# Performance work log

Measured on AMD Instinct MI355X. Metric: run time of the kernel, lower is better.

The kernel has to match this reference:

```python
import jax, jax.numpy as jnp
import numpy as np

N = 50000
GAMMA = 0.1

def spmm(row, col, val, x):
    # sparse [N,N] @ dense [N,D] via gather + segment-sum over destination rows
    return jax.ops.segment_sum(val[:, None] * x[col], row, num_segments=N)

def setup_inputs() -> dict:
    key = jax.random.key(0)
    ks = jax.random.split(key, 16)
    E, EK, F, H, C = 800000, 1000000, 512, 128, 40
    return {
        "fea": jax.random.normal(ks[0], (N, F), jnp.float32),
        "adj_row": jax.random.randint(ks[1], (E,), 0, N),
        "adj_col": jax.random.randint(ks[2], (E,), 0, N),
        "adj_val": jax.random.uniform(ks[3], (E,), jnp.float32),
        "knn_row": jax.random.randint(ks[4], (EK,), 0, N),
        "knn_col": jax.random.randint(ks[5], (EK,), 0, N),
        "knn_val": jax.random.uniform(ks[6], (EK,), jnp.float32),
        "W1": jax.random.normal(ks[7], (F, H), jnp.float32) * (1.0 / np.sqrt(F)),
        "b1": jnp.zeros((H,), jnp.float32),
        "W2": jax.random.normal(ks[8], (H, C), jnp.float32) * (1.0 / np.sqrt(H)),
        "b2": jnp.zeros((C,), jnp.float32),
        "score1": jax.random.normal(ks[9], (F, 1), jnp.float32),
        "score2": jax.random.normal(ks[10], (H, 1), jnp.float32),
        "sbias1": jnp.zeros((1,), jnp.float32),
        "sbias2": jnp.zeros((1,), jnp.float32),
        "Dk1": jax.random.normal(ks[11], (F, 1), jnp.float32),
        "Dk2": jax.random.normal(ks[12], (H, 1), jnp.float32),
        "Dbias1": jnp.zeros((1,), jnp.float32),
        "Dbias2": jnp.zeros((1,), jnp.float32),
    }

def simpgcn_layer(x, W, b, s_w, s_b, d_w, d_b, adj_row, adj_col, adj_val, knn_row, knn_col, knn_val):
    support = x @ W                     # [N, Dout] shared across the 3 adjacencies
    h_adj = spmm(adj_row, adj_col, adj_val, support) + b
    h_knn = spmm(knn_row, knn_col, knn_val, support) + b
    h_id = support + b                  # identity adjacency: spmm(I, support)
    s = jax.nn.sigmoid(x @ s_w + s_b)   # [N,1] learned self-loop gate
    Dk = x @ d_w + d_b                  # [N,1]
    return s * h_adj + (1.0 - s) * h_knn + GAMMA * Dk * h_id

def reference(fea, adj_row, adj_col, adj_val, knn_row, knn_col, knn_val,
              W1, b1, W2, b2, score1, score2, sbias1, sbias2,
              Dk1, Dk2, Dbias1, Dbias2):
    x = simpgcn_layer(fea, W1, b1, score1, sbias1, Dk1, Dbias1,
                      adj_row, adj_col, adj_val, knn_row, knn_col, knn_val)
    embedding = x  # dropout is identity in eval mode
    x = simpgcn_layer(x, W2, b2, score2, sbias2, Dk2, Dbias2,
                      adj_row, adj_col, adj_val, knn_row, knn_col, knn_val)
    return jax.nn.log_softmax(x, axis=1), embedding
```

## Files before the change

kernel.cpp:

```cpp
#include <hip/hip_runtime.h>
#include <hip/hip_bf16.h>
#include <cstdint>

#define GAMMA 0.1f
#define CAP 64
#define OVF_CAP 8192

typedef unsigned int  uint32;
typedef unsigned short ushort16;
typedef float f32x4 __attribute__((ext_vector_type(4)));
typedef __bf16 bf16x8 __attribute__((ext_vector_type(8)));

union U16x8 { uint4 u4; bf16x8 bv; };

static __device__ __forceinline__ ushort16 f2bf(float f) {
    union { float f; uint32 u; } x; x.f = f;
    uint32 r = (x.u + 0x7FFFu + ((x.u >> 16) & 1u)) >> 16;
    return (ushort16)r;
}
static __device__ __forceinline__ uint32 pack2bf(float lo, float hi) {
    return (uint32)f2bf(lo) | ((uint32)f2bf(hi) << 16);
}
static __device__ __forceinline__ float bflo(uint32 u) { return __uint_as_float(u << 16); }
static __device__ __forceinline__ float bfhi(uint32 u) { return __uint_as_float(u & 0xFFFF0000u); }

__global__ __launch_bounds__(256) void prep_wt(const float* __restrict__ W1,
                                               const float* __restrict__ W2,
                                               ushort16* __restrict__ W1bt,
                                               ushort16* __restrict__ W2bt) {
    int t = blockIdx.x * 256 + threadIdx.x;
    if (t < 128 * 512) { int c = t >> 9, k = t & 511; W1bt[t] = f2bf(W1[k * 128 + c]); }
    if (t < 48 * 128)  { int c = t >> 7, k = t & 127; W2bt[t] = f2bf(c < 40 ? W2[k * 40 + c] : 0.f); }
}

__global__ __launch_bounds__(256) void gemm1_scatter(
    const float* __restrict__ A, const ushort16* __restrict__ Bt,
    const float* __restrict__ s1w, const float* __restrict__ d1w,
    const float* __restrict__ s1b, const float* __restrict__ d1b,
    ushort16* __restrict__ Cb, float* __restrict__ s_out, float* __restrict__ dk_out,
    int M, int mgrid,
    const int* __restrict__ arow_, const int* __restrict__ acol_, const float* __restrict__ aval_, int E,
    const int* __restrict__ krow_, const int* __restrict__ kcol_, const float* __restrict__ kval_, int EK,
    int* __restrict__ cnt, int N,
    uint32* __restrict__ packed_a, uint32* __restrict__ packed_k,
    uint2* __restrict__ ovf_a, uint2* __restrict__ ovf_k) {
    int bid = blockIdx.x;
    if (bid >= mgrid) {
        int i = (bid - mgrid) * 256 + threadIdx.x;
        if (i < E) {
            int r = arow_[i];
            uint32 rec = ((uint32)acol_[i] << 16) | (uint32)f2bf(aval_[i]);
            int p = atomicAdd(&cnt[r], 1);
            if (p < CAP) packed_a[(size_t)r * CAP + p] = rec;
            else { int q = atomicAdd(&cnt[2 * N], 1); if (q < OVF_CAP) ovf_a[q] = make_uint2((uint32)r, rec); }
        }
        if (i < EK) {
            int r = krow_[i];
            uint32 rec = ((uint32)kcol_[i] << 16) | (uint32)f2bf(kval_[i]);
            int p = atomicAdd(&cnt[N + r], 1);
            if (p < CAP) packed_k[(size_t)r * CAP + p] = rec;
            else { int q = atomicAdd(&cnt[2 * N + 1], 1); if (q < OVF_CAP) ovf_k[q] = make_uint2((uint32)r, rec); }
        }
        return;
    }
    int w = threadIdx.x >> 6, lane = threadIdx.x & 63;
    int row16 = lane & 15, kc = lane >> 4;
    int wrow0 = bid * 64 + w * 16;
    int r = wrow0 + row16;
    int rc = min(r, M - 1);
    const float* arow = A + (size_t)rc * 512;

    f32x4 acc[8];
    #pragma unroll
    for (int c = 0; c < 8; ++c) acc[c] = (f32x4){0.f, 0.f, 0.f, 0.f};
    float sdot = 0.f, ddot = 0.f;

    for (int ks = 0; ks < 16; ++ks) {
        int kb = ks * 32 + kc * 8;
        float4 a0 = *reinterpret_cast<const float4*>(arow + kb);
        float4 a1 = *reinterpret_cast<const float4*>(arow + kb + 4);
        float4 sw0 = *reinterpret_cast<const float4*>(s1w + kb);
        float4 sw1 = *reinterpret_cast<const float4*>(s1w + kb + 4);
        float4 dw0 = *reinterpret_cast<const float4*>(d1w + kb);
        float4 dw1 = *reinterpret_cast<const float4*>(d1w + kb + 4);
        sdot += a0.x * sw0.x + a0.y * sw0.y + a0.z * sw0.z + a0.w * sw0.w +
                a1.x * sw1.x + a1.y * sw1.y + a1.z * sw1.z + a1.w * sw1.w;
        ddot += a0.x * dw0.x + a0.y * dw0.y + a0.z * dw0.z + a0.w * dw0.w +
                a1.x * dw1.x + a1.y * dw1.y + a1.z * dw1.z + a1.w * dw1.w;
        U16x8 ua;
        ua.u4 = make_uint4(pack2bf(a0.x, a0.y), pack2bf(a0.z, a0.w),
                           pack2bf(a1.x, a1.y), pack2bf(a1.z, a1.w));
        #pragma unroll
        for (int c = 0; c < 8; ++c) {
            U16x8 ub;
            ub.u4 = *reinterpret_cast<const uint4*>(Bt + (size_t)(c * 16 + row16) * 512 + kb);
            acc[c] = __builtin_amdgcn_mfma_f32_16x16x32_bf16(ua.bv, ub.bv, acc[c], 0, 0, 0);
        }
    }

    sdot += __shfl_xor(sdot, 16); sdot += __shfl_xor(sdot, 32);
    ddot += __shfl_xor(ddot, 16); ddot += __shfl_xor(ddot, 32);
    if (kc == 0 && r < M) {
        s_out[r] = 1.f / (1.f + __expf(-(sdot + s1b[0])));
        dk_out[r] = ddot + d1b[0];
    }

    #pragma unroll
    for (int c = 0; c < 8; ++c) {
        #pragma unroll
        for (int i = 0; i < 4; ++i) {
            int orow = wrow0 + (lane >> 4) * 4 + i;
            if (orow < M) Cb[(size_t)orow * 128 + c * 16 + row16] = f2bf(acc[c][i]);
        }
    }
}

__global__ __launch_bounds__(256) void gemm2_mfma(const ushort16* __restrict__ Ab,
                                                  const ushort16* __restrict__ Bt,
                                                  float* __restrict__ C,
                                                  ushort16* __restrict__ Cb,
                                                  int M) {
    int w = threadIdx.x >> 6, lane = threadIdx.x & 63;
    int row16 = lane & 15, kc = lane >> 4;
    int wrow0 = blockIdx.x * 64 + w * 16;
    int r = wrow0 + row16;
    int rc = min(r, M - 1);

    f32x4 acc[3];
    #pragma unroll
    for (int c = 0; c < 3; ++c) acc[c] = (f32x4){0.f, 0.f, 0.f, 0.f};

    #pragma unroll
    for (int ks = 0; ks < 4; ++ks) {
        int kb = ks * 32 + kc * 8;
        U16x8 ua;
        ua.u4 = *reinterpret_cast<const uint4*>(Ab + (size_t)rc * 128 + kb);
        #pragma unroll
        for (int c = 0; c < 3; ++c) {
            U16x8 ub;
            ub.u4 = *reinterpret_cast<const uint4*>(Bt + (size_t)(c * 16 + row16) * 128 + kb);
            acc[c] = __builtin_amdgcn_mfma_f32_16x16x32_bf16(ua.bv, ub.bv, acc[c], 0, 0, 0);
        }
    }

    #pragma unroll
    for (int c = 0; c < 3; ++c) {
        int col = c * 16 + row16;
        #pragma unroll
        for (int i = 0; i < 4; ++i) {
            int orow = wrow0 + (lane >> 4) * 4 + i;
            if (orow < M && col < 40) {
                C[(size_t)orow * 40 + col] = acc[c][i];
                Cb[(size_t)orow * 40 + col] = f2bf(acc[c][i]);
            }
        }
    }
}

__global__ __launch_bounds__(256) void spmm_combine1(
    const int* __restrict__ cnt,
    const uint32* __restrict__ packed_a, const uint32* __restrict__ packed_k,
    const uint2* __restrict__ ovf_a, const uint2* __restrict__ ovf_k,
    const ushort16* __restrict__ supb, const float* __restrict__ s, const float* __restrict__ dk,
    const float* __restrict__ b1,
    const float* __restrict__ s2w, const float* __restrict__ d2w,
    const float* __restrict__ s2b, const float* __restrict__ d2b,
    float* __restrict__ emb, ushort16* __restrict__ embb,
    float* __restrict__ s_out, float* __restrict__ dk_out, int N) {
    int w = threadIdx.x >> 6, lane = threadIdx.x & 63;
    int r = blockIdx.x * 4 + w;
    if (r >= N) return;
    const uint32* su = (const uint32*)supb;

    float a0 = 0.f, a1 = 0.f, k0 = 0.f, k1 = 0.f;
    {
        const uint32* pa = packed_a + (size_t)r * CAP;
        int d = min(cnt[r], CAP);
        int e = 0;
        for (; e + 2 <= d; e += 2) {
            uint32 r0 = pa[e], r1 = pa[e + 1];
            float v0 = bflo(r0), v1 = bflo(r1);
            uint32 u0 = su[((size_t)(r0 >> 16) << 6) + lane];
            uint32 u1 = su[((size_t)(r1 >> 16) << 6) + lane];
            a0 += v0 * bflo(u0) + v1 * bflo(u1);
            a1 += v0 * bfhi(u0) + v1 * bfhi(u1);
        }
        if (e < d) {
            uint32 r0 = pa[e];
            float v0 = bflo(r0);
            uint32 u0 = su[((size_t)(r0 >> 16) << 6) + lane];
            a0 += v0 * bflo(u0); a1 += v0 * bfhi(u0);
        }
    }
    {
        const uint32* pk = packed_k + (size_t)r * CAP;
        int d = min(cnt[N + r], CAP);
        int e = 0;
        for (; e + 2 <= d; e += 2) {
            uint32 r0 = pk[e], r1 = pk[e + 1];
            float v0 = bflo(r0), v1 = bflo(r1);
            uint32 u0 = su[((size_t)(r0 >> 16) << 6) + lane];
            uint32 u1 = su[((size_t)(r1 >> 16) << 6) + lane];
            k0 += v0 * bflo(u0) + v1 * bflo(u1);
            k1 += v0 * bfhi(u0) + v1 * bfhi(u1);
        }
        if (e < d) {
            uint32 r0 = pk[e];
            float v0 = bflo(r0);
            uint32 u0 = su[((size_t)(r0 >> 16) << 6) + lane];
            k0 += v0 * bflo(u0); k1 += v0 * bfhi(u0);
        }
    }
    int nova = min(cnt[2 * N], OVF_CAP);
    for (int i = 0; i < nova; ++i) {
        uint2 t = ovf_a[i];
        if ((int)t.x == r) {
            float v = bflo(t.y);
            uint32 u = su[((size_t)(t.y >> 16) << 6) + lane];
            a0 += v * bflo(u); a1 += v * bfhi(u);
        }
    }
    int novk = min(cnt[2 * N + 1], OVF_CAP);
    for (int i = 0; i < novk; ++i) {
        uint2 t = ovf_k[i];
        if ((int)t.x == r) {
            float v = bflo(t.y);
            uint32 u = su[((size_t)(t.y >> 16) << 6) + lane];
            k0 += v * bflo(u); k1 += v * bfhi(u);
        }
    }

    float si = s[r];
    float g = GAMMA * dk[r];
    uint32 ui = su[((size_t)r << 6) + lane];
    int c0i = lane * 2, c1i = lane * 2 + 1;
    float o0 = si * a0 + (1.f - si) * k0 + g * bflo(ui) + b1[c0i] * (1.f + g);
    float o1 = si * a1 + (1.f - si) * k1 + g * bfhi(ui) + b1[c1i] * (1.f + g);

    *reinterpret_cast<float2*>(emb + (size_t)r * 128 + c0i) = make_float2(o0, o1);
    ((uint32*)embb)[((size_t)r << 6) + lane] = pack2bf(o0, o1);

    float as = o0 * s2w[c0i] + o1 * s2w[c1i];
    float ad = o0 * d2w[c0i] + o1 * d2w[c1i];
    #pragma unroll
    for (int off = 32; off; off >>= 1) {
        as += __shfl_xor(as, off);
        ad += __shfl_xor(ad, off);
    }
    if (lane == 0) {
        s_out[r] = 1.f / (1.f + __expf(-(as + s2b[0])));
        dk_out[r] = ad + d2b[0];
    }
}

__global__ __launch_bounds__(256) void spmm_combine2_lsm(
    const int* __restrict__ cnt,
    const uint32* __restrict__ packed_a, const uint32* __restrict__ packed_k,
    const uint2* __restrict__ ovf_a, const uint2* __restrict__ ovf_k,
    const ushort16* __restrict__ supb, const float* __restrict__ supf,
    const float* __restrict__ s, const float* __restrict__ dk,
    const float* __restrict__ b2, float* __restrict__ out, int N) {
    int w = threadIdx.x >> 6, lane = threadIdx.x & 63;
    int r = blockIdx.x * 4 + w;
    if (r >= N) return;
    int g = lane >> 5, li = lane & 31;
    bool act = li < 20;
    const uint32* su = (const uint32*)supb;

    float a0 = 0.f, a1 = 0.f, k0 = 0.f, k1 = 0.f;
    {
        const uint32* pa = packed_a + (size_t)r * CAP;
        int d = min(cnt[r], CAP);
        for (int e = g; e < d; e += 2) {
            uint32 rec = pa[e];
            float v = bflo(rec);
            if (act) {
                uint32 u = su[(size_t)(rec >> 16) * 20 + li];
                a0 += v * bflo(u); a1 += v * bfhi(u);
            }
        }
    }
    {
        const uint32* pk = packed_k + (size_t)r * CAP;
        int d = min(cnt[N + r], CAP);
        for (int e = g; e < d; e += 2) {
            uint32 rec = pk[e];
            float v = bflo(rec);
            if (act) {
                uint32 u = su[(size_t)(rec >> 16) * 20 + li];
                k0 += v * bflo(u); k1 += v * bfhi(u);
            }
        }
    }
    int nova = min(cnt[2 * N], OVF_CAP);
    for (int i = 0; i < nova; ++i) {
        uint2 t = ovf_a[i];
        if ((int)t.x == r && g == 0 && act) {
            float v = bflo(t.y);
            uint32 u = su[(size_t)(t.y >> 16) * 20 + li];
            a0 += v * bflo(u); a1 += v * bfhi(u);
        }
    }
    int novk = min(cnt[2 * N + 1], OVF_CAP);
    for (int i = 0; i < novk; ++i) {
        uint2 t = ovf_k[i];
        if ((int)t.x == r && g == 0 && act) {
            float v = bflo(t.y);
            uint32 u = su[(size_t)(t.y >> 16) * 20 + li];
            k0 += v * bflo(u); k1 += v * bfhi(u);
        }
    }
    a0 += __shfl_xor(a0, 32); a1 += __shfl_xor(a1, 32);
    k0 += __shfl_xor(k0, 32); k1 += __shfl_xor(k1, 32);

    float si = s[r];
    float gg = GAMMA * dk[r];
    float z0 = -INFINITY, z1 = -INFINITY;
    bool lead = act && (lane < 32);
    if (lead) {
        float2 iv = *reinterpret_cast<const float2*>(supf + (size_t)r * 40 + li * 2);
        z0 = si * a0 + (1.f - si) * k0 + gg * iv.x + b2[li * 2] * (1.f + gg);
        z1 = si * a1 + (1.f - si) * k1 + gg * iv.y + b2[li * 2 + 1] * (1.f + gg);
    }
    float m = fmaxf(z0, z1);
    #pragma unroll
    for (int off = 16; off; off >>= 1) m = fmaxf(m, __shfl_xor(m, off));
    float ex = lead ? (__expf(z0 - m) + __expf(z1 - m)) : 0.f;
    #pragma unroll
    for (int off = 16; off; off >>= 1) ex += __shfl_xor(ex, off);
    float lse = m + __logf(ex);
    if (lead)
        *reinterpret_cast<float2*>(out + (size_t)r * 40 + li * 2) = make_float2(z0 - lse, z1 - lse);
}

static inline size_t align256(size_t x) { return (x + 255) & ~(size_t)255; }

extern "C" void kernel_launch(void* const* d_in, const int* in_sizes, int n_in,
                              void* d_out, int out_size, void* d_ws, size_t ws_size,
                              hipStream_t stream) {
    const int N = 50000, C = 40;

    const float* fea     = (const float*)d_in[0];
    const int*   adj_row = (const int*)d_in[1];
    const int*   adj_col = (const int*)d_in[2];
    const float* adj_val = (const float*)d_in[3];
    const int*   knn_row = (const int*)d_in[4];
    const int*   knn_col = (const int*)d_in[5];
    const float* knn_val = (const float*)d_in[6];
    const float* W1      = (const float*)d_in[7];
    const float* b1      = (const float*)d_in[8];
    const float* W2      = (const float*)d_in[9];
    const float* b2      = (const float*)d_in[10];
    const float* score1  = (const float*)d_in[11];
    const float* score2  = (const float*)d_in[12];
    const float* sbias1  = (const float*)d_in[13];
    const float* sbias2  = (const float*)d_in[14];
    const float* Dk1     = (const float*)d_in[15];
    const float* Dk2     = (const float*)d_in[16];
    const float* Dbias1  = (const float*)d_in[17];
    const float* Dbias2  = (const float*)d_in[18];

    const int E  = in_sizes[1];
    const int EK = in_sizes[4];

    float* out_lsm = (float*)d_out;
    float* emb     = out_lsm + (size_t)N * C;

    char* wp = (char*)d_ws;
    ushort16* W1bt = (ushort16*)wp; wp += align256((size_t)128 * 512 * 2);
    ushort16* W2bt = (ushort16*)wp; wp += align256((size_t)48 * 128 * 2);
    char* sup1_region = wp;          wp += align256((size_t)N * 128 * 2);
    ushort16* sup1b = (ushort16*)sup1_region;
    float* sup2     = (float*)sup1_region;
    ushort16* sup2b = (ushort16*)(sup1_region + (size_t)N * 40 * 4);
    ushort16* embb  = (ushort16*)wp; wp += align256((size_t)N * 128 * 2);
    float* s_buf  = (float*)wp; wp += align256((size_t)N * 4);
    float* dk_buf = (float*)wp; wp += align256((size_t)N * 4);
    int* cnt  = (int*)wp; wp += align256((size_t)(2 * N + 2) * 4);
    uint32* packed_a = (uint32*)wp; wp += align256((size_t)N * CAP * 4);
    uint32* packed_k = (uint32*)wp; wp += align256((size_t)N * CAP * 4);
    uint2* ovf_a = (uint2*)wp; wp += align256((size_t)OVF_CAP * 8);
    uint2* ovf_k = (uint2*)wp; wp += align256((size_t)OVF_CAP * 8);

    int egrid = (max(E, EK) + 255) / 256;
    int mgrid = (N + 63) / 64;

    prep_wt<<<256, 256, 0, stream>>>(W1, W2, W1bt, W2bt);
    hipMemsetAsync(cnt, 0, (size_t)(2 * N + 2) * 4, stream);

    gemm1_scatter<<<mgrid + egrid, 256, 0, stream>>>(
        fea, W1bt, score1, Dk1, sbias1, Dbias1, sup1b, s_buf, dk_buf, N, mgrid,
        adj_row, adj_col, adj_val, E, knn_row, knn_col, knn_val, EK,
        cnt, N, packed_a, packed_k, ovf_a, ovf_k);

    spmm_combine1<<<(N + 3) / 4, 256, 0, stream>>>(cnt, packed_a, packed_k, ovf_a, ovf_k,
                                                   sup1b, s_buf, dk_buf, b1,
                                                   score2, Dk2, sbias2, Dbias2,
                                                   emb, embb, s_buf, dk_buf, N);

    gemm2_mfma<<<mgrid, 256, 0, stream>>>(embb, W2bt, sup2, sup2b, N);

    spmm_combine2_lsm<<<(N + 3) / 4, 256, 0, stream>>>(cnt, packed_a, packed_k, ovf_a, ovf_k,
                                                       sup2b, sup2, s_buf, dk_buf,
                                                       b2, out_lsm, N);

    (void)n_in; (void)out_size; (void)ws_size;
}
```

Baseline: 538.0 us.

## Bin edges by 4-row groups with sub-bins to cut atomic contention

Replaces per-row adjacency/knn buckets with shared bins per group of 4 rows, split into 8 sub-bins by block to spread atomic contention, storing col, row-offset and matrix tag per record. The SpMM kernels now process one bin group per block, with each wave taking strided records, accumulating into 16 per-row/per-matrix registers, and reducing across waves through shared memory. Counter zeroing moves from a memset into prep_wt. The per-record switch, the LDS reduction and a larger overflow list scanned by every row add cost, and the 16-bit row field in the overflow record truncates row indices above 65535.

```diff
diff --git a/kernel.cpp b/kernel.cpp
--- a/kernel.cpp
+++ b/kernel.cpp
@@ -3,8 +3,10 @@
 #include <cstdint>
 
 #define GAMMA 0.1f
-#define CAP 64
-#define OVF_CAP 8192
+#define NBINS 12500
+#define NSUB 8
+#define CAPS 32
+#define OVF_CAP 16384
 
 typedef unsigned int  uint32;
 typedef unsigned short ushort16;
@@ -27,10 +29,12 @@
 __global__ __launch_bounds__(256) void prep_wt(const float* __restrict__ W1,
                                                const float* __restrict__ W2,
                                                ushort16* __restrict__ W1bt,
-                                               ushort16* __restrict__ W2bt) {
+                                               ushort16* __restrict__ W2bt,
+                                               int* __restrict__ bcnt) {
     int t = blockIdx.x * 256 + threadIdx.x;
     if (t < 128 * 512) { int c = t >> 9, k = t & 511; W1bt[t] = f2bf(W1[k * 128 + c]); }
     if (t < 48 * 128)  { int c = t >> 7, k = t & 127; W2bt[t] = f2bf(c < 40 ? W2[k * 40 + c] : 0.f); }
+    for (int j = t; j < NBINS * NSUB + 1; j += 256 * 256) bcnt[j] = 0;
 }
 
 __global__ __launch_bounds__(256) void gemm1_scatter(
@@ -41,25 +45,37 @@
     int M, int mgrid,
     const int* __restrict__ arow_, const int* __restrict__ acol_, const float* __restrict__ aval_, int E,
     const int* __restrict__ krow_, const int* __restrict__ kcol_, const float* __restrict__ kval_, int EK,
-    int* __restrict__ cnt, int N,
-    uint32* __restrict__ packed_a, uint32* __restrict__ packed_k,
-    uint2* __restrict__ ovf_a, uint2* __restrict__ ovf_k) {
+    int* __restrict__ bcnt, uint2* __restrict__ bins, uint2* __restrict__ ovf) {
     int bid = blockIdx.x;
     if (bid >= mgrid) {
         int i = (bid - mgrid) * 256 + threadIdx.x;
+        int sub = bid & (NSUB - 1);
+        int* ovf_cnt = bcnt + NBINS * NSUB;
         if (i < E) {
             int r = arow_[i];
-            uint32 rec = ((uint32)acol_[i] << 16) | (uint32)f2bf(aval_[i]);
-            int p = atomicAdd(&cnt[r], 1);
-            if (p < CAP) packed_a[(size_t)r * CAP + p] = rec;
-            else { int q = atomicAdd(&cnt[2 * N], 1); if (q < OVF_CAP) ovf_a[q] = make_uint2((uint32)r, rec); }
+            int col = acol_[i];
+            uint32 vb = (uint32)f2bf(aval_[i]);
+            int slot = (r >> 2) * NSUB + sub;
+            int p = atomicAdd(&bcnt[slot], 1);
+            uint32 rx = (uint32)col | ((uint32)(r & 3) << 16);
+            if (p < CAPS) bins[(size_t)slot * CAPS + p] = make_uint2(rx, vb);
+            else {
+                int q = atomicAdd(ovf_cnt, 1);
+                if (q < OVF_CAP) ovf[q] = make_uint2((uint32)r, (uint32)col | (vb << 16));
+            }
         }
         if (i < EK) {
             int r = krow_[i];
-            uint32 rec = ((uint32)kcol_[i] << 16) | (uint32)f2bf(kval_[i]);
-            int p = atomicAdd(&cnt[N + r], 1);
-            if (p < CAP) packed_k[(size_t)r * CAP + p] = rec;
-            else { int q = atomicAdd(&cnt[2 * N + 1], 1); if (q < OVF_CAP) ovf_k[q] = make_uint2((uint32)r, rec); }
+            int col = kcol_[i];
+            uint32 vb = (uint32)f2bf(kval_[i]);
+            int slot = (r >> 2) * NSUB + sub;
+            int p = atomicAdd(&bcnt[slot], 1);
+            uint32 rx = (uint32)col | ((uint32)(r & 3) << 16) | (1u << 18);
+            if (p < CAPS) bins[(size_t)slot * CAPS + p] = make_uint2(rx, vb);
+            else {
+                int q = atomicAdd(ovf_cnt, 1);
+                if (q < OVF_CAP) ovf[q] = make_uint2((uint32)r | 0x10000u, (uint32)col | (vb << 16));
+            }
         }
         return;
     }
@@ -158,87 +174,84 @@
 }
 
 __global__ __launch_bounds__(256) void spmm_combine1(
-    const int* __restrict__ cnt,
-    const uint32* __restrict__ packed_a, const uint32* __restrict__ packed_k,
-    const uint2* __restrict__ ovf_a, const uint2* __restrict__ ovf_k,
+    const int* __restrict__ bcnt, const uint2* __restrict__ bins,
+    const uint2* __restrict__ ovf,
     const ushort16* __restrict__ supb, const float* __restrict__ s, const float* __restrict__ dk,
     const float* __restrict__ b1,
     const float* __restrict__ s2w, const float* __restrict__ d2w,
     const float* __restrict__ s2b, const float* __restrict__ d2b,
     float* __restrict__ emb, ushort16* __restrict__ embb,
-    float* __restrict__ s_out, float* __restrict__ dk_out, int N) {
-    int w = threadIdx.x >> 6, lane = threadIdx.x & 63;
-    int r = blockIdx.x * 4 + w;
-    if (r >= N) return;
+    float* __restrict__ s_out, float* __restrict__ dk_out) {
+    int b = blockIdx.x;
+    int w = threadIdx.x >> 6, l = threadIdx.x & 63;
     const uint32* su = (const uint32*)supb;
 
-    float a0 = 0.f, a1 = 0.f, k0 = 0.f, k1 = 0.f;
-    {
-        const uint32* pa = packed_a + (size_t)r * CAP;
-        int d = min(cnt[r], CAP);
-        int e = 0;
-        for (; e + 2 <= d; e += 2) {
-            uint32 r0 = pa[e], r1 = pa[e + 1];
-            float v0 = bflo(r0), v1 = bflo(r1);
-            uint32 u0 = su[((size_t)(r0 >> 16) << 6) + lane];
-            uint32 u1 = su[((size_t)(r1 >> 16) << 6) + lane];
-            a0 += v0 * bflo(u0) + v1 * bflo(u1);
-            a1 += v0 * bfhi(u0) + v1 * bfhi(u1);
-        }
-        if (e < d) {
-            uint32 r0 = pa[e];
-            float v0 = bflo(r0);
-            uint32 u0 = su[((size_t)(r0 >> 16) << 6) + lane];
-            a0 += v0 * bflo(u0); a1 += v0 * bfhi(u0);
-        }
-    }
-    {
-        const uint32* pk = packed_k + (size_t)r * CAP;
-        int d = min(cnt[N + r], CAP);
-        int e = 0;
-        for (; e + 2 <= d; e += 2) {
-            uint32 r0 = pk[e], r1 = pk[e + 1];
-            float v0 = bflo(r0), v1 = bflo(r1);
-            uint32 u0 = su[((size_t)(r0 >> 16) << 6) + lane];
-            uint32 u1 = su[((size_t)(r1 >> 16) << 6) + lane];
-            k0 += v0 * bflo(u0) + v1 * bflo(u1);
-            k1 += v0 * bfhi(u0) + v1 * bfhi(u1);
-        }
-        if (e < d) {
-            uint32 r0 = pk[e];
-            float v0 = bflo(r0);
-            uint32 u0 = su[((size_t)(r0 >> 16) << 6) + lane];
-            k0 += v0 * bflo(u0); k1 += v0 * bfhi(u0);
-        }
-    }
-    int nova = min(cnt[2 * N], OVF_CAP);
-    for (int i = 0; i < nova; ++i) {
-        uint2 t = ovf_a[i];
-        if ((int)t.x == r) {
-            float v = bflo(t.y);
-            uint32 u = su[((size_t)(t.y >> 16) << 6) + lane];
-            a0 += v * bflo(u); a1 += v * bfhi(u);
-        }
-    }
-    int novk = min(cnt[2 * N + 1], OVF_CAP);
-    for (int i = 0; i < novk; ++i) {
-        uint2 t = ovf_k[i];
-        if ((int)t.x == r) {
-            float v = bflo(t.y);
-            uint32 u = su[((size_t)(t.y >> 16) << 6) + lane];
-            k0 += v * bflo(u); k1 += v * bfhi(u);
-        }
+    float a00=0,a01=0,a10=0,a11=0,a20=0,a21=0,a30=0,a31=0;
+    float k00=0,k01=0,k10=0,k11=0,k20=0,k21=0,k30=0,k31=0;
+
+#define PROC1(rec) { \
+    uint32 rx = __builtin_amdgcn_readfirstlane((rec).x); \
+    uint32 ry = __builtin_amdgcn_readfirstlane((rec).y); \
+    float v = bflo(ry); \
+    uint32 u = su[((size_t)(rx & 0xFFFFu) << 6) + l]; \
+    float g0 = v * bflo(u), g1 = v * bfhi(u); \
+    switch ((rx >> 16) & 7u) { \
+      case 0: a00+=g0; a01+=g1; break; \
+      case 1: a10+=g0; a11+=g1; break; \
+      case 2: a20+=g0; a21+=g1; break; \
+      case 3: a30+=g0; a31+=g1; break; \
+      case 4: k00+=g0; k01+=g1; break; \
+      case 5: k10+=g0; k11+=g1; break; \
+      case 6: k20+=g0; k21+=g1; break; \
+      default: k30+=g0; k31+=g1; break; \
+    } }
+
+    for (int sub = 0; sub < NSUB; ++sub) {
+        int slot = b * NSUB + sub;
+        const uint2* bp = bins + (size_t)slot * CAPS;
+        int d = min(bcnt[slot], CAPS);
+        int e = w;
+        for (; e + 4 < d; e += 8) { uint2 rA = bp[e]; uint2 rB = bp[e + 4]; PROC1(rA); PROC1(rB); }
+        for (; e < d; e += 4) { uint2 rA = bp[e]; PROC1(rA); }
+    }
+#undef PROC1
+
+    __shared__ float red[4][16][64];
+    red[w][0][l]=a00;  red[w][1][l]=a01;  red[w][2][l]=a10;  red[w][3][l]=a11;
+    red[w][4][l]=a20;  red[w][5][l]=a21;  red[w][6][l]=a30;  red[w][7][l]=a31;
+    red[w][8][l]=k00;  red[w][9][l]=k01;  red[w][10][l]=k10; red[w][11][l]=k11;
+    red[w][12][l]=k20; red[w][13][l]=k21; red[w][14][l]=k30; red[w][15][l]=k31;
+    __syncthreads();
+
+    float accA0=0, accA1=0, accK0=0, accK1=0;
+    #pragma unroll
+    for (int wv = 0; wv < 4; ++wv) {
+        accA0 += red[wv][w*2+0][l];
+        accA1 += red[wv][w*2+1][l];
+        accK0 += red[wv][8+w*2+0][l];
+        accK1 += red[wv][8+w*2+1][l];
+    }
+
+    int r = b * 4 + w;
+    int nov = min(bcnt[NBINS * NSUB], OVF_CAP);
+    for (int i = 0; i < nov; ++i) {
+        uint2 t = ovf[i];
+        if ((int)(t.x & 0xFFFFu) != r) continue;
+        float v = bfhi(t.y);
+        uint32 u = su[((size_t)(t.y & 0xFFFFu) << 6) + l];
+        if (t.x & 0x10000u) { accK0 += v * bflo(u); accK1 += v * bfhi(u); }
+        else                { accA0 += v * bflo(u); accA1 += v * bfhi(u); }
     }
 
     float si = s[r];
     float g = GAMMA * dk[r];
-    uint32 ui = su[((size_t)r << 6) + lane];
-    int c0i = lane * 2, c1i = lane * 2 + 1;
-    float o0 = si * a0 + (1.f - si) * k0 + g * bflo(ui) + b1[c0i] * (1.f + g);
-    float o1 = si * a1 + (1.f - si) * k1 + g * bfhi(ui) + b1[c1i] * (1.f + g);
+    uint32 ui = su[((size_t)r << 6) + l];
+    int c0i = l * 2, c1i = l * 2 + 1;
+    float o0 = si * accA0 + (1.f - si) * accK0 + g * bflo(ui) + b1[c0i] * (1.f + g);
+    float o1 = si * accA1 + (1.f - si) * accK1 + g * bfhi(ui) + b1[c1i] * (1.f + g);
 
     *reinterpret_cast<float2*>(emb + (size_t)r * 128 + c0i) = make_float2(o0, o1);
-    ((uint32*)embb)[((size_t)r << 6) + lane] = pack2bf(o0, o1);
+    ((uint32*)embb)[((size_t)r << 6) + l] = pack2bf(o0, o1);
 
     float as = o0 * s2w[c0i] + o1 * s2w[c1i];
     float ad = o0 * d2w[c0i] + o1 * d2w[c1i];
@@ -247,90 +260,102 @@
         as += __shfl_xor(as, off);
         ad += __shfl_xor(ad, off);
     }
-    if (lane == 0) {
+    if (l == 0) {
         s_out[r] = 1.f / (1.f + __expf(-(as + s2b[0])));
         dk_out[r] = ad + d2b[0];
     }
 }
 
 __global__ __launch_bounds__(256) void spmm_combine2_lsm(
-    const int* __restrict__ cnt,
-    const uint32* __restrict__ packed_a, const uint32* __restrict__ packed_k,
-    const uint2* __restrict__ ovf_a, const uint2* __restrict__ ovf_k,
+    const int* __restrict__ bcnt, const uint2* __restrict__ bins,
+    const uint2* __restrict__ ovf,
     const ushort16* __restrict__ supb, const float* __restrict__ supf,
     const float* __restrict__ s, const float* __restrict__ dk,
-    const float* __restrict__ b2, float* __restrict__ out, int N) {
-    int w = threadIdx.x >> 6, lane = threadIdx.x & 63;
-    int r = blockIdx.x * 4 + w;
-    if (r >= N) return;
-    int g = lane >> 5, li = lane & 31;
-    bool act = li < 20;
+    const float* __restrict__ b2, float* __restrict__ out) {
+    int b = blockIdx.x;
+    int w = threadIdx.x >> 6, l = threadIdx.x & 63;
+    bool act = l < 20;
     const uint32* su = (const uint32*)supb;
 
-    float a0 = 0.f, a1 = 0.f, k0 = 0.f, k1 = 0.f;
-    {
-        const uint32* pa = packed_a + (size_t)r * CAP;
-        int d = min(cnt[r], CAP);
-        for (int e = g; e < d; e += 2) {
-            uint32 rec = pa[e];
-            float v = bflo(rec);
-            if (act) {
-                uint32 u = su[(size_t)(rec >> 16) * 20 + li];
-                a0 += v * bflo(u); a1 += v * bfhi(u);
-            }
-        }
-    }
-    {
-        const uint32* pk = packed_k + (size_t)r * CAP;
-        int d = min(cnt[N + r], CAP);
-        for (int e = g; e < d; e += 2) {
-            uint32 rec = pk[e];
-            float v = bflo(rec);
-            if (act) {
-                uint32 u = su[(size_t)(rec >> 16) * 20 + li];
-                k0 += v * bflo(u); k1 += v * bfhi(u);
-            }
-        }
-    }
-    int nova = min(cnt[2 * N], OVF_CAP);
-    for (int i = 0; i < nova; ++i) {
-        uint2 t = ovf_a[i];
-        if ((int)t.x == r && g == 0 && act) {
-            float v = bflo(t.y);
-            uint32 u = su[(size_t)(t.y >> 16) * 20 + li];
-            a0 += v * bflo(u); a1 += v * bfhi(u);
-        }
-    }
-    int novk = min(cnt[2 * N + 1], OVF_CAP);
-    for (int i = 0; i < novk; ++i) {
-        uint2 t = ovf_k[i];
-        if ((int)t.x == r && g == 0 && act) {
-            float v = bflo(t.y);
-            uint32 u = su[(size_t)(t.y >> 16) * 20 + li];
-            k0 += v * bflo(u); k1 += v * bfhi(u);
-        }
-    }
-    a0 += __shfl_xor(a0, 32); a1 += __shfl_xor(a1, 32);
-    k0 += __shfl_xor(k0, 32); k1 += __shfl_xor(k1, 32);
+    float a00=0,a01=0,a10=0,a11=0,a20=0,a21=0,a30=0,a31=0;
+    float k00=0,k01=0,k10=0,k11=0,k20=0,k21=0,k30=0,k31=0;
+
+#define PROC2(rec) { \
+    uint32 rx = __builtin_amdgcn_readfirstlane((rec).x); \
+    uint32 ry = __builtin_amdgcn_readfirstlane((rec).y); \
+    float v = bflo(ry); \
+    float g0 = 0.f, g1 = 0.f; \
+    if (act) { \
+        uint32 u = su[(size_t)(rx & 0xFFFFu) * 20 + l]; \
+        g0 = v * bflo(u); g1 = v * bfhi(u); \
+    } \
+    switch ((rx >> 16) & 7u) { \
+      case 0: a00+=g0; a01+=g1; break; \
+      case 1: a10+=g0; a11+=g1; break; \
+      case 2: a20+=g0; a21+=g1; break; \
+      case 3: a30+=g0; a31+=g1; break; \
+      case 4: k00+=g0; k01+=g1; break; \
+      case 5: k10+=g0; k11+=g1; break; \
+      case 6: k20+=g0; k21+=g1; break; \
+      default: k30+=g0; k31+=g1; break; \
+    } }
+
+    for (int sub = 0; sub < NSUB; ++sub) {
+        int slot = b * NSUB + sub;
+        const uint2* bp = bins + (size_t)slot * CAPS;
+        int d = min(bcnt[slot], CAPS);
+        int e = w;
+        for (; e + 4 < d; e += 8) { uint2 rA = bp[e]; uint2 rB = bp[e + 4]; PROC2(rA); PROC2(rB); }
+        for (; e < d; e += 4) { uint2 rA = bp[e]; PROC2(rA); }
+    }
+#undef PROC2
+
+    __shared__ float red[4][16][64];
+    red[w][0][l]=a00;  red[w][1][l]=a01;  red[w][2][l]=a10;  red[w][3][l]=a11;
+    red[w][4][l]=a20;  red[w][5][l]=a21;  red[w][6][l]=a30;  red[w][7][l]=a31;
+    red[w][8][l]=k00;  red[w][9][l]=k01;  red[w][10][l]=k10; red[w][11][l]=k11;
+    red[w][12][l]=k20; red[w][13][l]=k21; red[w][14][l]=k30; red[w][15][l]=k31;
+    __syncthreads();
+
+    float accA0=0, accA1=0, accK0=0, accK1=0;
+    #pragma unroll
+    for (int wv = 0; wv < 4; ++wv) {
+        accA0 += red[wv][w*2+0][l];
+        accA1 += red[wv][w*2+1][l];
+        accK0 += red[wv][8+w*2+0][l];
+        accK1 += red[wv][8+w*2+1][l];
+    }
+
+    int r = b * 4 + w;
+    int nov = min(bcnt[NBINS * NSUB], OVF_CAP);
+    for (int i = 0; i < nov; ++i) {
+        uint2 t = ovf[i];
+        if ((int)(t.x & 0xFFFFu) != r) continue;
+        float v = bfhi(t.y);
+        if (act) {
+            uint32 u = su[(size_t)(t.y & 0xFFFFu) * 20 + l];
+            if (t.x & 0x10000u) { accK0 += v * bflo(u); accK1 += v * bfhi(u); }
+            else                { accA0 += v * bflo(u); accA1 += v * bfhi(u); }
+        }
+    }
 
     float si = s[r];
     float gg = GAMMA * dk[r];
     float z0 = -INFINITY, z1 = -INFINITY;
-    bool lead = act && (lane < 32);
-    if (lead) {
-        float2 iv = *reinterpret_cast<const float2*>(supf + (size_t)r * 40 + li * 2);
-        z0 = si * a0 + (1.f - si) * k0 + gg * iv.x + b2[li * 2] * (1.f + gg);
-        z1 = si * a1 + (1.f - si) * k1 + gg * iv.y + b2[li * 2 + 1] * (1.f + gg);
+    if (act) {
+        float2 iv = *reinterpret_cast<const float2*>(supf + (size_t)r * 40 + l * 2);
+        z0 = si * accA0 + (1.f - si) * accK0 + gg * iv.x + b2[l * 2] * (1.f + gg);
+        z1 = si * accA1 + (1.f - si) * accK1 + gg * iv.y + b2[l * 2 + 1] * (1.f + gg);
     }
     float m = fmaxf(z0, z1);
     #pragma unroll
     for (int off = 16; off; off >>= 1) m = fmaxf(m, __shfl_xor(m, off));
-    float ex = lead ? (__expf(z0 - m) + __expf(z1 - m)) : 0.f;
+    float ex = act ? (__expf(z0 - m) + __expf(z1 - m)) : 0.f;
     #pragma unroll
     for (int off = 16; off; off >>= 1) ex += __shfl_xor(ex, off);
     float lse = m + __logf(ex);
-    if (lead)
-        *reinterpret_cast<float2*>(out + (size_t)r * 40 + li * 2) = make_float2(z0 - lse, z1 - lse);
+    if (act)
+        *reinterpret_cast<float2*>(out + (size_t)r * 40 + l * 2) = make_float2(z0 - lse, z1 - lse);
 }
 
 static inline size_t align256(size_t x) { return (x + 255) & ~(size_t)255; }
@@ -376,33 +401,30 @@
     ushort16* embb  = (ushort16*)wp; wp += align256((size_t)N * 128 * 2);
     float* s_buf  = (float*)wp; wp += align256((size_t)N * 4);
     float* dk_buf = (float*)wp; wp += align256((size_t)N * 4);
-    int* cnt  = (int*)wp; wp += align256((size_t)(2 * N + 2) * 4);
-    uint32* packed_a = (uint32*)wp; wp += align256((size_t)N * CAP * 4);
-    uint32* packed_k = (uint32*)wp; wp += align256((size_t)N * CAP * 4);
-    uint2* ovf_a = (uint2*)wp; wp += align256((size_t)OVF_CAP * 8);
-    uint2* ovf_k = (uint2*)wp; wp += align256((size_t)OVF_CAP * 8);
+    int* bcnt = (int*)wp; wp += align256((size_t)(NBINS * NSUB + 1) * 4);
+    uint2* bins = (uint2*)wp; wp += align256((size_t)NBINS * NSUB * CAPS * 8);
+    uint2* ovf  = (uint2*)wp; wp += align256((size_t)OVF_CAP * 8);
 
     int egrid = (max(E, EK) + 255) / 256;
     int mgrid = (N + 63) / 64;
 
-    prep_wt<<<256, 256, 0, stream>>>(W1, W2, W1bt, W2bt);
-    hipMemsetAsync(cnt, 0, (size_t)(2 * N + 2) * 4, stream);
+    prep_wt<<<256, 256, 0, stream>>>(W1, W2, W1bt, W2bt, bcnt);
 
     gemm1_scatter<<<mgrid + egrid, 256, 0, stream>>>(
         fea, W1bt, score1, Dk1, sbias1, Dbias1, sup1b, s_buf, dk_buf, N, mgrid,
         adj_row, adj_col, adj_val, E, knn_row, knn_col, knn_val, EK,
-        cnt, N, packed_a, packed_k, ovf_a, ovf_k);
-
-    spmm_combine1<<<(N + 3) / 4, 256, 0, stream>>>(cnt, packed_a, packed_k, ovf_a, ovf_k,
-                                                   sup1b, s_buf, dk_buf, b1,
-                                                   score2, Dk2, sbias2, Dbias2,
-                                                   emb, embb, s_buf, dk_buf, N);
+        bcnt, bins, ovf);
+
+    spmm_combine1<<<NBINS, 256, 0, stream>>>(bcnt, bins, ovf,
+                                             sup1b, s_buf, dk_buf, b1,
+                                             score2, Dk2, sbias2, Dbias2,
+                                             emb, embb, s_buf, dk_buf);
 
     gemm2_mfma<<<mgrid, 256, 0, stream>>>(embb, W2bt, sup2, sup2b, N);
 
-    spmm_combine2_lsm<<<(N + 3) / 4, 256, 0, stream>>>(cnt, packed_a, packed_k, ovf_a, ovf_k,
-                                                       sup2b, sup2, s_buf, dk_buf,
-                                                       b2, out_lsm, N);
+    spmm_combine2_lsm<<<NBINS, 256, 0, stream>>>(bcnt, bins, ovf,
+                                                 sup2b, sup2, s_buf, dk_buf,
+                                                 b2, out_lsm);
 
     (void)n_in; (void)out_size; (void)ws_size;
 }
```

New measurement: 875.4 us. 62.7% more time.
